# Performance work log

Hardware: AMD Instinct MI355X
Metric: run time of the kernel (lower is better)

The kernel has to match this reference:

```python
import jax, jax.numpy as jnp
import numpy as np

# dims
B, S, A = 16384, 300, 30
EMB, M_TOK, M_PROTO = 256, 8, 16
H_ENC, H_DEC, MF, NZ = 256, 128, 12, 4
ALPHA_MIN, ALPHA_MAX, ETA0 = 0.06, 0.3, 0.1
TECH_IDX = jnp.array([61, 91, 121, 151, 181, 211, 241, 271])


def setup_inputs() -> dict:
    key = jax.random.key(0)
    ks = jax.random.split(key, 20)
    def w(k, shape, fan):
        return jax.random.normal(k, shape, jnp.float32) * (fan ** -0.5)
    return {
        'state':   jax.random.uniform(ks[0], (B, S), jnp.float32),
        'fitness': jax.random.uniform(ks[1], (B, M_PROTO), jnp.float32),
        'proto_keys': jax.random.normal(ks[2], (M_PROTO, EMB), jnp.float32) * (EMB ** -0.5),
        'enc_W1': w(ks[3], (S, H_ENC), S),   'enc_b1': jnp.zeros((H_ENC,), jnp.float32),
        'ln_g':   jnp.ones((H_ENC,), jnp.float32), 'ln_b': jnp.zeros((H_ENC,), jnp.float32),
        'enc_W2': w(ks[4], (H_ENC, M_TOK * EMB), H_ENC), 'enc_b2': jnp.zeros((M_TOK * EMB,), jnp.float32),
        'dec_W1': w(ks[5], (M_PROTO, EMB, H_DEC), EMB),  'dec_b1': jnp.zeros((M_PROTO, H_DEC), jnp.float32),
        'dec_W2': w(ks[6], (M_PROTO, H_DEC, A), H_DEC),  'dec_b2': jnp.zeros((M_PROTO, A), jnp.float32),
        'tc_W':  w(ks[7], (MF, EMB), MF),  'tc_b':  jnp.zeros((EMB,), jnp.float32),
        'tc_cW': w(ks[8], (EMB, 1), EMB),  'tc_cb': jnp.zeros((1,), jnp.float32),
        'tc_zW': w(ks[9], (EMB, NZ), EMB), 'tc_zb': jnp.zeros((NZ,), jnp.float32),
        'w_prev': jnp.full((1, M_PROTO), 1.0 / M_PROTO, jnp.float32),
    }


def _layernorm(x, g, b, eps=1e-5):
    mu = x.mean(-1, keepdims=True)
    var = ((x - mu) ** 2).mean(-1, keepdims=True)
    return (x - mu) * jax.lax.rsqrt(var + eps) * g + b


def _forward(state, fitness, proto_keys, enc_W1, enc_b1, ln_g, ln_b, enc_W2, enc_b2,
             dec_W1, dec_b1, dec_W2, dec_b2, tc_W, tc_b, tc_cW, tc_cb, tc_zW, tc_zb, w_prev):
    # --- market feature extraction ---
    balance = state[:, 0:1]
    prices = state[:, 1:31]
    shares = state[:, 31:61]
    price_mean = prices.mean(1, keepdims=True)
    price_std = jnp.std(prices, axis=1, keepdims=True, ddof=1) + 1e-8  # torch.std is unbiased
    total_value = balance + (prices * shares).sum(1, keepdims=True)
    cash_ratio = balance / (total_value + 1e-8)
    tech = state[:, TECH_IDX]
    mf = jnp.concatenate([balance, price_mean, price_std, cash_ratio, tech], axis=1)  # [B,12]
    # --- T-Cell (minimal surrogate: danger embed, crisis level, crisis types) ---
    danger = jnp.tanh(mf @ tc_W + tc_b)                     # [B,EMB]
    crisis = jax.nn.sigmoid(danger @ tc_cW + tc_cb)         # [B,1]
    z = jax.nn.softmax(danger @ tc_zW + tc_zb, axis=-1)     # [B,NZ]
    # --- epitope encoder: Linear -> LN -> ReLU -> Linear -> reshape [B,m,EMB] ---
    h = jax.nn.relu(_layernorm(state @ enc_W1 + enc_b1, ln_g, ln_b))
    E = (h @ enc_W2 + enc_b2).reshape(-1, M_TOK, EMB)
    # --- IRT routing (OT-attention + fitness replicator, crisis-gated mix) ---
    scale = EMB ** -0.5
    logits = jnp.einsum('bme,ne->bmn', E, proto_keys) * scale \
           + (jnp.einsum('be,ne->bn', danger, proto_keys) * scale)[:, None, :]  # [B,m,M]
    P = jax.nn.softmax(logits, axis=-1)
    w_ot = P.mean(axis=1)                                   # [B,M]
    w_rep = w_prev * jnp.exp(ETA0 * fitness)
    w_rep = w_rep / (w_rep.sum(-1, keepdims=True) + 1e-8)
    alpha_c = ALPHA_MIN + (ALPHA_MAX - ALPHA_MIN) * (1.0 - crisis)  # [B,1]
    w = alpha_c * w_ot + (1.0 - alpha_c) * w_rep
    w = w / (w.sum(-1, keepdims=True) + 1e-8)
    # --- per-expert decoders on proto_keys (batched GEMM over M experts) ---
    hd = jax.nn.relu(jnp.einsum('me,meh->mh', proto_keys, dec_W1) + dec_b1)
    conc = jax.nn.softplus(jnp.einsum('mh,mha->ma', hd, dec_W2) + dec_b2)  # [M,A]
    mixed = jnp.einsum('bm,ma->ba', w, conc) + 1.0          # [B,A]
    # deterministic branch: softmax action head
    action = jax.nn.softmax(mixed, axis=-1)
    action = jnp.clip(action, 0.0, 1.0)
    action = action / (action.sum(-1, keepdims=True) + 1e-8)
    return action


def reference(state, fitness, proto_keys, enc_W1, enc_b1, ln_g, ln_b, enc_W2, enc_b2,
              dec_W1, dec_b1, dec_W2, dec_b2, tc_W, tc_b, tc_cW, tc_cb, tc_zW, tc_zb, w_prev):
    return _forward(state, fitness, proto_keys, enc_W1, enc_b1, ln_g, ln_b, enc_W2, enc_b2,
                    dec_W1, dec_b1, dec_W2, dec_b2, tc_W, tc_b, tc_cW, tc_cb, tc_zW, tc_zb, w_prev)
```

## Files before the change

kernel.cpp:

```cpp
#include <hip/hip_runtime.h>

typedef __attribute__((ext_vector_type(8))) short bf16x8;
typedef __attribute__((ext_vector_type(4))) float f32x4;

#define NBATCH 16384
#define SS     300
#define AA     30
#define ROWS   16
#define SSTR   352
#define HSTR   280
#define LSTR   132
#define K1P    320
#define SCALEF 0.0625f
#define ETA0   0.1f

__device__ __forceinline__ short f2b(float x) {
    unsigned u = __float_as_uint(x);
    unsigned r = (u + 0x7FFFu + ((u >> 16) & 1u)) >> 16;
    return (short)r;
}
__device__ __forceinline__ float b2f(short s) {
    return __uint_as_float(((unsigned)(unsigned short)s) << 16);
}
__device__ __forceinline__ float tanh_fast(float x) {
    float e = __expf(2.f * x);
    return 1.f - 2.f / (e + 1.f);
}

__global__ __launch_bounds__(256) void pre_kernel(
    const float* __restrict__ proto, const float* __restrict__ W1,
    const float* __restrict__ W2,   const float* __restrict__ b2,
    const float* __restrict__ tcW,  const float* __restrict__ cWp,
    const float* __restrict__ dW1,  const float* __restrict__ db1,
    const float* __restrict__ dW2,  const float* __restrict__ db2,
    short* __restrict__ W1P, short* __restrict__ W3P,
    short* __restrict__ PDP, short* __restrict__ TCP,
    float* __restrict__ cmn, float* __restrict__ conc)
{
    __shared__ short sbuf[64 * 264 + 4096];
    const int t = threadIdx.x;
    const int bid = blockIdx.x;

    if (bid < 32) {
        const int m = bid >> 2, jt = bid & 3;
        short* W2s = sbuf;
        short* prS = sbuf + 64 * 264;
        #pragma unroll 8
        for (int it = 0; it < 64; ++it) {
            const int idx = it * 256 + t, j = idx >> 8, e = idx & 255;
            W2s[j * 264 + e] = f2b(W2[(size_t)(jt * 64 + j) * 2048 + m * 256 + e]);
        }
        #pragma unroll 8
        for (int it = 0; it < 16; ++it) {
            const int id = it * 256 + t, chunk = id >> 3, j8 = id & 7;
            const int kt = chunk >> 6, rem = chunk & 63, q = rem >> 4, n = rem & 15;
            prS[id] = f2b(proto[n * 256 + kt * 32 + q * 8 + j8]);
        }
        __syncthreads();
        const int lane = t & 63, wv = t >> 6, l15 = lane & 15, q = lane >> 4;
        f32x4 acc = {0.f, 0.f, 0.f, 0.f};
        for (int kt = 0; kt < 8; ++kt) {
            bf16x8 a = *(const bf16x8*)&W2s[(wv * 16 + l15) * 264 + kt * 32 + q * 8];
            bf16x8 b = *(const bf16x8*)&prS[((kt * 4 + q) * 16 + l15) * 8];
            acc = __builtin_amdgcn_mfma_f32_16x16x32_bf16(a, b, acc, 0, 0, 0);
        }
        #pragma unroll
        for (int reg = 0; reg < 4; ++reg) {
            const int jg = jt * 64 + wv * 16 + q * 4 + reg;
            const int c = m * 16 + l15;
            const int ktj = jg >> 5, qj = (jg >> 3) & 3, j8 = jg & 7;
            W3P[((ktj * 4 + qj) * 128 + c) * 8 + j8] = f2b(acc[reg]);
        }
    } else if (bid < 42) {
        const int kt = bid - 32;
        short* W1s = sbuf;
        #pragma unroll 8
        for (int it = 0; it < 32; ++it) {
            const int idx = it * 256 + t, k = idx >> 8, n = idx & 255;
            const int kg = kt * 32 + k;
            W1s[k * 256 + n] = (kg < SS) ? f2b(W1[(size_t)kg * 256 + n]) : (short)0;
        }
        __syncthreads();
        #pragma unroll
        for (int it = 0; it < 4; ++it) {
            const int id = it * 256 + t, q = id >> 8, n = id & 255;
            bf16x8 v;
            #pragma unroll
            for (int j = 0; j < 8; ++j) v[j] = W1s[(q * 8 + j) * 256 + n];
            *(bf16x8*)&W1P[((kt * 4 + q) * 256 + n) * 8] = v;
        }
    } else if (bid == 42) {
        #pragma unroll 4
        for (int it = 0; it < 32; ++it) {
            const int id = it * 256 + t, chunk = id >> 3, j8 = id & 7;
            const int kt = chunk >> 7, q = (chunk >> 5) & 3, np = chunk & 31;
            const int k = kt * 32 + q * 8 + j8;
            float v = 0.f;
            if (np < 16) v = proto[np * 256 + k];
            else if (np == 16) v = cWp[k];
            PDP[id] = f2b(v);
        }
    } else if (bid == 43) {
        #pragma unroll 4
        for (int it = 0; it < 32; ++it) {
            const int id = it * 256 + t, chunk = id >> 3, j8 = id & 7;
            const int q = chunk >> 8, n = chunk & 255, k = q * 8 + j8;
            TCP[id] = (k < 12) ? f2b(tcW[k * 256 + n]) : (short)0;
        }
    } else if (bid == 44) {
        float* b2s = (float*)sbuf;
        float* prF = b2s + 2048;
        #pragma unroll
        for (int it = 0; it < 8; ++it)  b2s[it * 256 + t] = b2[it * 256 + t];
        #pragma unroll
        for (int it = 0; it < 16; ++it) prF[it * 256 + t] = proto[it * 256 + t];
        __syncthreads();
        if (t < 128) {
            const int mq = t >> 4, n = t & 15;
            float acc = 0.f;
            #pragma unroll 4
            for (int e = 0; e < 256; ++e) acc += b2s[mq * 256 + e] * prF[n * 256 + e];
            cmn[t] = acc;
        }
    } else {
        const int m = bid - 45;
        float* pr    = (float*)sbuf;
        float* hdp   = pr + 256;
        float* hdv   = hdp + 256;
        float* cpart = hdv + 128;
        pr[t] = proto[m * 256 + t];
        __syncthreads();
        {
            const int half = t >> 7, h = t & 127;
            const float* wp = dW1 + (size_t)m * 32768 + (size_t)half * 16384 + h;
            float a0 = 0.f, a1 = 0.f, a2 = 0.f, a3 = 0.f;
            #pragma unroll 8
            for (int e = 0; e < 128; e += 4) {
                const int eg = half * 128 + e;
                a0 = fmaf(pr[eg + 0], wp[(e + 0) * 128], a0);
                a1 = fmaf(pr[eg + 1], wp[(e + 1) * 128], a1);
                a2 = fmaf(pr[eg + 2], wp[(e + 2) * 128], a2);
                a3 = fmaf(pr[eg + 3], wp[(e + 3) * 128], a3);
            }
            hdp[half * 128 + h] = (a0 + a1) + (a2 + a3);
        }
        __syncthreads();
        if (t < 128) hdv[t] = fmaxf(hdp[t] + hdp[128 + t] + db1[m * 128 + t], 0.f);
        __syncthreads();
        {
            const int g = t >> 5, a = t & 31;
            float cacc = 0.f;
            if (a < AA) {
                const float* w2p = dW2 + (size_t)m * 128 * AA + g * 16 * AA + a;
                #pragma unroll
                for (int hh = 0; hh < 16; ++hh)
                    cacc = fmaf(hdv[g * 16 + hh], w2p[hh * AA], cacc);
            }
            cpart[g * 32 + a] = cacc;
        }
        __syncthreads();
        if (t < AA) {
            float s = db2[m * AA + t];
            #pragma unroll
            for (int g2 = 0; g2 < 8; ++g2) s += cpart[g2 * 32 + t];
            conc[m * AA + t] = fmaxf(s, 0.f) + log1pf(__expf(-fabsf(s)));
        }
    }
}

__global__ __launch_bounds__(256, 5) void main_kernel(
    const float* __restrict__ state, const float* __restrict__ fitness,
    const float* __restrict__ b1,
    const float* __restrict__ lng,  const float* __restrict__ lnb,
    const float* __restrict__ tcb,  const float* __restrict__ cb,
    const float* __restrict__ pw,
    const short* __restrict__ W1P,  const short* __restrict__ W3P,
    const short* __restrict__ PDP,  const short* __restrict__ TCP,
    const float* __restrict__ cmn,  const float* __restrict__ conc,
    float* __restrict__ out)
{
    const int t    = threadIdx.x;
    const int row0 = blockIdx.x * ROWS;
    const int w    = t >> 6;
    const int lane = t & 63;
    const int l15  = lane & 15;
    const int q    = lane >> 4;

    __shared__ short sA[ROWS * SSTR];
    __shared__ short sB[ROWS * HSTR];
    __shared__ short s_mfB[ROWS * 32];
    __shared__ float s_red[ROWS][8];
    __shared__ float s_mu[ROWS], s_rstd[ROWS];
    __shared__ float s_dd[ROWS * 16];
    __shared__ float s_crisis[ROWS];
    __shared__ float s_cmn[128];
    __shared__ float s_conc[16 * AA];

    float* s_log  = (float*)sB;
    float* s_wrep = (float*)&sA[ROWS * HSTR];

    #pragma unroll 4
    for (int it = 0; it < 20; ++it) {
        const int idx = it * 256 + t, r = idx / K1P, k = idx - r * K1P;
        sA[r * SSTR + k] = (k < SS) ? f2b(state[(size_t)(row0 + r) * SS + k]) : (short)0;
    }
    for (int it = t; it < 128 + 16 * AA; it += 256) {
        if (it < 128) s_cmn[it] = cmn[it];
        else s_conc[it - 128] = conc[it - 128];
    }
    __syncthreads();

    {
        const int r = t >> 4, g = t & 15;
        float sp = 0.f, sp2 = 0.f, sps = 0.f;
        if (g < 15) {
            #pragma unroll
            for (int jj = 0; jj < 2; ++jj) {
                const int i = 2 * g + jj;
                const float p = b2f(sA[r * SSTR + 1 + i]);
                const float s = b2f(sA[r * SSTR + 31 + i]);
                sp += p; sp2 += p * p; sps += p * s;
            }
        }
        #pragma unroll
        for (int off = 1; off < 16; off <<= 1) {
            sp  += __shfl_xor(sp, off);
            sp2 += __shfl_xor(sp2, off);
            sps += __shfl_xor(sps, off);
        }
        if (g < 8) s_mfB[r * 32 + 4 + g] = sA[r * SSTR + 61 + 30 * g];
        for (int k = 12 + g; k < 32; k += 16) s_mfB[r * 32 + k] = 0;
        if (g == 0) {
            const float bal = b2f(sA[r * SSTR]);
            const float pm = sp * (1.f / 30.f);
            const float var = (sp2 - 30.f * pm * pm) * (1.f / 29.f);
            const float pstd = sqrtf(fmaxf(var, 0.f)) + 1e-8f;
            s_mfB[r * 32 + 0] = sA[r * SSTR];
            s_mfB[r * 32 + 1] = f2b(pm);
            s_mfB[r * 32 + 2] = f2b(pstd);
            s_mfB[r * 32 + 3] = f2b(bal / (bal + sps + 1e-8f));
        }
    }
    __syncthreads();

    {
        f32x4 dacc[4];
        #pragma unroll
        for (int u = 0; u < 4; ++u) dacc[u] = (f32x4){0.f, 0.f, 0.f, 0.f};
        bf16x8 a = *(const bf16x8*)&s_mfB[l15 * 32 + q * 8];
        #pragma unroll
        for (int u = 0; u < 4; ++u) {
            bf16x8 b = *(const bf16x8*)&TCP[((q << 8) | (w * 64 + u * 16 + l15)) * 8];
            dacc[u] = __builtin_amdgcn_mfma_f32_16x16x32_bf16(a, b, dacc[u], 0, 0, 0);
        }
        #pragma unroll
        for (int u = 0; u < 4; ++u) {
            const int col = w * 64 + u * 16 + l15;
            const float tb = tcb[col];
            #pragma unroll
            for (int reg = 0; reg < 4; ++reg)
                sB[(q * 4 + reg) * HSTR + col] = f2b(tanh_fast(dacc[u][reg] + tb));
        }
    }
    __syncthreads();

    if (w == 0) {
        f32x4 acc = {0.f, 0.f, 0.f, 0.f};
        for (int kt = 0; kt < 8; ++kt) {
            bf16x8 a = *(const bf16x8*)&sB[l15 * HSTR + kt * 32 + q * 8];
            bf16x8 b = *(const bf16x8*)&PDP[((kt * 4 + q) * 32 + l15) * 8];
            acc = __builtin_amdgcn_mfma_f32_16x16x32_bf16(a, b, acc, 0, 0, 0);
        }
        #pragma unroll
        for (int reg = 0; reg < 4; ++reg)
            s_dd[(q * 4 + reg) * 16 + l15] = acc[reg];
    } else if (w == 1) {
        f32x4 acc = {0.f, 0.f, 0.f, 0.f};
        for (int kt = 0; kt < 8; ++kt) {
            bf16x8 a = *(const bf16x8*)&sB[l15 * HSTR + kt * 32 + q * 8];
            bf16x8 b = *(const bf16x8*)&PDP[((kt * 4 + q) * 32 + 16 + l15) * 8];
            acc = __builtin_amdgcn_mfma_f32_16x16x32_bf16(a, b, acc, 0, 0, 0);
        }
        if (l15 == 0) {
            const float cbv = cb[0];
            #pragma unroll
            for (int reg = 0; reg < 4; ++reg)
                s_crisis[q * 4 + reg] = 1.f / (1.f + __expf(-(acc[reg] + cbv)));
        }
    }

    f32x4 acc[4];
    #pragma unroll
    for (int u = 0; u < 4; ++u) acc[u] = (f32x4){0.f, 0.f, 0.f, 0.f};
    for (int kt = 0; kt < 10; ++kt) {
        bf16x8 a = *(const bf16x8*)&sA[l15 * SSTR + kt * 32 + q * 8];
        bf16x8 bfr[4];
        #pragma unroll
        for (int u = 0; u < 4; ++u)
            bfr[u] = *(const bf16x8*)&W1P[((kt * 4 + q) * 256 + (w * 64 + u * 16 + l15)) * 8];
        #pragma unroll
        for (int u = 0; u < 4; ++u)
            acc[u] = __builtin_amdgcn_mfma_f32_16x16x32_bf16(a, bfr[u], acc[u], 0, 0, 0);
    }

    {
        float b1v[4];
        #pragma unroll
        for (int u = 0; u < 4; ++u) b1v[u] = b1[w * 64 + u * 16 + l15];
        #pragma unroll
        for (int reg = 0; reg < 4; ++reg) {
            float s = 0.f, s2 = 0.f;
            #pragma unroll
            for (int u = 0; u < 4; ++u) {
                const float v = acc[u][reg] + b1v[u];
                acc[u][reg] = v;
                s += v; s2 += v * v;
            }
            #pragma unroll
            for (int off = 1; off < 16; off <<= 1) {
                s  += __shfl_xor(s, off);
                s2 += __shfl_xor(s2, off);
            }
            if (l15 == 0) {
                const int row = q * 4 + reg;
                s_red[row][w * 2]     = s;
                s_red[row][w * 2 + 1] = s2;
            }
        }
    }
    __syncthreads();
    if (t < ROWS) {
        float S = 0.f, S2 = 0.f;
        #pragma unroll
        for (int ww = 0; ww < 4; ++ww) { S += s_red[t][2 * ww]; S2 += s_red[t][2 * ww + 1]; }
        const float mu = S * (1.f / 256.f);
        const float var = S2 * (1.f / 256.f) - mu * mu;
        s_mu[t] = mu; s_rstd[t] = rsqrtf(var + 1e-5f);
    }
    __syncthreads();

    {
        float gv[4], bv[4];
        #pragma unroll
        for (int u = 0; u < 4; ++u) {
            gv[u] = lng[w * 64 + u * 16 + l15];
            bv[u] = lnb[w * 64 + u * 16 + l15];
        }
        #pragma unroll
        for (int reg = 0; reg < 4; ++reg) {
            const int row = q * 4 + reg;
            const float mu = s_mu[row], rs = s_rstd[row];
            #pragma unroll
            for (int u = 0; u < 4; ++u) {
                const int col = w * 64 + u * 16 + l15;
                const float v = fmaxf((acc[u][reg] - mu) * rs * gv[u] + bv[u], 0.f);
                sA[row * HSTR + col] = f2b(v);
            }
        }
    }
    __syncthreads();

    {
        f32x4 c2[2];
        c2[0] = (f32x4){0.f, 0.f, 0.f, 0.f};
        c2[1] = (f32x4){0.f, 0.f, 0.f, 0.f};
        for (int kt = 0; kt < 8; ++kt) {
            bf16x8 a = *(const bf16x8*)&sA[l15 * HSTR + kt * 32 + q * 8];
            bf16x8 b0 = *(const bf16x8*)&W3P[((kt * 4 + q) * 128 + w * 32 + l15) * 8];
            bf16x8 b1f = *(const bf16x8*)&W3P[((kt * 4 + q) * 128 + w * 32 + 16 + l15) * 8];
            c2[0] = __builtin_amdgcn_mfma_f32_16x16x32_bf16(a, b0, c2[0], 0, 0, 0);
            c2[1] = __builtin_amdgcn_mfma_f32_16x16x32_bf16(a, b1f, c2[1], 0, 0, 0);
        }
        const float cm0 = s_cmn[w * 32 + l15], cm1 = s_cmn[w * 32 + 16 + l15];
        #pragma unroll
        for (int reg = 0; reg < 4; ++reg) {
            const int row = q * 4 + reg;
            const float dd = s_dd[row * 16 + l15];
            s_log[row * LSTR + w * 32 + l15]      = SCALEF * (c2[0][reg] + cm0 + dd);
            s_log[row * LSTR + w * 32 + 16 + l15] = SCALEF * (c2[1][reg] + cm1 + dd);
        }
    }
    __syncthreads();

    if (t < 128) {
        const int r = t >> 3, m = t & 7;
        float* lg = &s_log[r * LSTR + m * 16];
        float mx = lg[0];
        #pragma unroll
        for (int n = 1; n < 16; ++n) mx = fmaxf(mx, lg[n]);
        float sum = 0.f, p[16];
        #pragma unroll
        for (int n = 0; n < 16; ++n) { p[n] = __expf(lg[n] - mx); sum += p[n]; }
        const float inv = 1.f / sum;
        #pragma unroll
        for (int n = 0; n < 16; ++n) lg[n] = p[n] * inv;
    }
    __syncthreads();

    {
        const int r = t >> 4, n = t & 15;
        float wot = 0.f;
        #pragma unroll
        for (int m = 0; m < 8; ++m) wot += s_log[r * LSTR + m * 16 + n];
        s_dd[t] = wot * 0.125f;
        s_wrep[t] = pw[n] * __expf(ETA0 * fitness[(size_t)(row0 + r) * 16 + n]);
    }
    __syncthreads();

    if (t < ROWS) {
        float srep = 0.f;
        #pragma unroll
        for (int n = 0; n < 16; ++n) srep += s_wrep[t * 16 + n];
        const float irep = 1.f / (srep + 1e-8f);
        const float alpha = 0.06f + 0.24f * (1.f - s_crisis[t]);
        float wn[16], sw = 0.f;
        #pragma unroll
        for (int n = 0; n < 16; ++n) {
            wn[n] = alpha * s_dd[t * 16 + n] + (1.f - alpha) * s_wrep[t * 16 + n] * irep;
            sw += wn[n];
        }
        const float isw = 1.f / (sw + 1e-8f);
        #pragma unroll
        for (int n = 0; n < 16; ++n) s_dd[t * 16 + n] = wn[n] * isw;
    }
    __syncthreads();

    {
        const int r = w * 4 + q;
        const int a0 = l15;
        const int a1 = a0 + 16;
        const bool v1 = a1 < AA;
        float wreg[16];
        #pragma unroll
        for (int n = 0; n < 16; ++n) wreg[n] = s_dd[r * 16 + n];
        float m0 = 1.f, m1 = 1.f;
        const int a1s = v1 ? a1 : 0;
        #pragma unroll
        for (int n = 0; n < 16; ++n) {
            m0 = fmaf(wreg[n], s_conc[n * AA + a0], m0);
            m1 = fmaf(wreg[n], s_conc[n * AA + a1s], m1);
        }
        float mx = v1 ? fmaxf(m0, m1) : m0;
        #pragma unroll
        for (int off = 1; off < 16; off <<= 1) mx = fmaxf(mx, __shfl_xor(mx, off));
        float e0 = __expf(m0 - mx);
        float e1 = v1 ? __expf(m1 - mx) : 0.f;
        float se = e0 + e1;
        #pragma unroll
        for (int off = 1; off < 16; off <<= 1) se += __shfl_xor(se, off);
        const float inv = 1.f / se;
        out[(size_t)(row0 + r) * AA + a0] = e0 * inv;
        if (v1) out[(size_t)(row0 + r) * AA + a1] = e1 * inv;
    }
}

extern "C" void kernel_launch(void* const* d_in, const int* in_sizes, int n_in,
                              void* d_out, int out_size, void* d_ws, size_t ws_size,
                              hipStream_t stream) {
    const float* state   = (const float*)d_in[0];
    const float* fitness = (const float*)d_in[1];
    const float* proto   = (const float*)d_in[2];
    const float* enc_W1  = (const float*)d_in[3];
    const float* enc_b1  = (const float*)d_in[4];
    const float* ln_g    = (const float*)d_in[5];
    const float* ln_b    = (const float*)d_in[6];
    const float* enc_W2  = (const float*)d_in[7];
    const float* enc_b2  = (const float*)d_in[8];
    const float* dec_W1  = (const float*)d_in[9];
    const float* dec_b1  = (const float*)d_in[10];
    const float* dec_W2  = (const float*)d_in[11];
    const float* dec_b2  = (const float*)d_in[12];
    const float* tc_W    = (const float*)d_in[13];
    const float* tc_b    = (const float*)d_in[14];
    const float* tc_cW   = (const float*)d_in[15];
    const float* tc_cb   = (const float*)d_in[16];
    const float* w_prev  = (const float*)d_in[19];
    float* out = (float*)d_out;

    short* W1P = (short*)d_ws;
    short* W3P = W1P + 81920;
    short* PDP = W3P + 32768;
    short* TCP = PDP + 8192;
    float* cmn  = (float*)(TCP + 8192);
    float* conc = cmn + 128;

    pre_kernel<<<61, 256, 0, stream>>>(proto, enc_W1, enc_W2, enc_b2,
                                       tc_W, tc_cW,
                                       dec_W1, dec_b1, dec_W2, dec_b2,
                                       W1P, W3P, PDP, TCP, cmn, conc);
    main_kernel<<<NBATCH / ROWS, 256, 0, stream>>>(state, fitness,
                                                   enc_b1, ln_g, ln_b,
                                                   tc_b, tc_cb, w_prev,
                                                   W1P, W3P, PDP, TCP, cmn, conc, out);
}
```

Measured before the change: 132.8 us.

## Vectorize state load, prefetch fitness, overlap W1 GEMM, drop LN barrier

The state tile is now loaded as float4 with packed bf16 stores, and the shared row stride is shrunk to fit. Fitness and prior weights are prefetched at kernel entry so their global latency is hidden. The encoder W1 GEMM moves ahead of the barrier so it runs alongside the tech-context stage, and each thread recomputes the LayerNorm mean and rstd from the partial sums, removing one shared round trip and one __syncthreads. This costs extra register pressure and redundant per-thread reductions.

```diff
diff --git a/kernel.cpp b/kernel.cpp
--- a/kernel.cpp
+++ b/kernel.cpp
@@ -7,7 +7,7 @@
 #define SS     300
 #define AA     30
 #define ROWS   16
-#define SSTR   352
+#define SSTR   328
 #define HSTR   280
 #define LSTR   132
 #define K1P    320
@@ -190,7 +190,6 @@
     __shared__ short sB[ROWS * HSTR];
     __shared__ short s_mfB[ROWS * 32];
     __shared__ float s_red[ROWS][8];
-    __shared__ float s_mu[ROWS], s_rstd[ROWS];
     __shared__ float s_dd[ROWS * 16];
     __shared__ float s_crisis[ROWS];
     __shared__ float s_cmn[128];
@@ -199,10 +198,23 @@
     float* s_log  = (float*)sB;
     float* s_wrep = (float*)&sA[ROWS * HSTR];
 
-    #pragma unroll 4
-    for (int it = 0; it < 20; ++it) {
-        const int idx = it * 256 + t, r = idx / K1P, k = idx - r * K1P;
-        sA[r * SSTR + k] = (k < SS) ? f2b(state[(size_t)(row0 + r) * SS + k]) : (short)0;
+    const float fit_pre = fitness[(size_t)(row0 + (t >> 4)) * 16 + (t & 15)];
+    const float pw_pre  = pw[t & 15];
+
+    #pragma unroll
+    for (int it = 0; it < 5; ++it) {
+        const int idx = it * 256 + t;
+        if (idx < ROWS * 75) {
+            const int r = idx / 75, c4 = idx - r * 75;
+            const float4 v = *(const float4*)&state[(size_t)(row0 + r) * SS + c4 * 4];
+            short4 s4;
+            s4.x = f2b(v.x); s4.y = f2b(v.y); s4.z = f2b(v.z); s4.w = f2b(v.w);
+            *(short4*)&sA[r * SSTR + c4 * 4] = s4;
+        }
+    }
+    for (int i = t; i < ROWS * 20; i += 256) {
+        const int r = i / 20, k = SS + i - r * 20;
+        sA[r * SSTR + k] = 0;
     }
     for (int it = t; it < 128 + 16 * AA; it += 256) {
         if (it < 128) s_cmn[it] = cmn[it];
@@ -243,15 +255,16 @@
     }
     __syncthreads();
 
+    f32x4 acc[4];
     {
         f32x4 dacc[4];
         #pragma unroll
         for (int u = 0; u < 4; ++u) dacc[u] = (f32x4){0.f, 0.f, 0.f, 0.f};
-        bf16x8 a = *(const bf16x8*)&s_mfB[l15 * 32 + q * 8];
+        bf16x8 amf = *(const bf16x8*)&s_mfB[l15 * 32 + q * 8];
         #pragma unroll
         for (int u = 0; u < 4; ++u) {
             bf16x8 b = *(const bf16x8*)&TCP[((q << 8) | (w * 64 + u * 16 + l15)) * 8];
-            dacc[u] = __builtin_amdgcn_mfma_f32_16x16x32_bf16(a, b, dacc[u], 0, 0, 0);
+            dacc[u] = __builtin_amdgcn_mfma_f32_16x16x32_bf16(amf, b, dacc[u], 0, 0, 0);
         }
         #pragma unroll
         for (int u = 0; u < 4; ++u) {
@@ -261,48 +274,45 @@
             for (int reg = 0; reg < 4; ++reg)
                 sB[(q * 4 + reg) * HSTR + col] = f2b(tanh_fast(dacc[u][reg] + tb));
         }
+        #pragma unroll
+        for (int u = 0; u < 4; ++u) acc[u] = (f32x4){0.f, 0.f, 0.f, 0.f};
+        for (int kt = 0; kt < 10; ++kt) {
+            bf16x8 a = *(const bf16x8*)&sA[l15 * SSTR + kt * 32 + q * 8];
+            bf16x8 bfr[4];
+            #pragma unroll
+            for (int u = 0; u < 4; ++u)
+                bfr[u] = *(const bf16x8*)&W1P[((kt * 4 + q) * 256 + (w * 64 + u * 16 + l15)) * 8];
+            #pragma unroll
+            for (int u = 0; u < 4; ++u)
+                acc[u] = __builtin_amdgcn_mfma_f32_16x16x32_bf16(a, bfr[u], acc[u], 0, 0, 0);
+        }
     }
     __syncthreads();
 
     if (w == 0) {
-        f32x4 acc = {0.f, 0.f, 0.f, 0.f};
+        f32x4 ad = {0.f, 0.f, 0.f, 0.f};
         for (int kt = 0; kt < 8; ++kt) {
             bf16x8 a = *(const bf16x8*)&sB[l15 * HSTR + kt * 32 + q * 8];
             bf16x8 b = *(const bf16x8*)&PDP[((kt * 4 + q) * 32 + l15) * 8];
-            acc = __builtin_amdgcn_mfma_f32_16x16x32_bf16(a, b, acc, 0, 0, 0);
+            ad = __builtin_amdgcn_mfma_f32_16x16x32_bf16(a, b, ad, 0, 0, 0);
         }
         #pragma unroll
         for (int reg = 0; reg < 4; ++reg)
-            s_dd[(q * 4 + reg) * 16 + l15] = acc[reg];
+            s_dd[(q * 4 + reg) * 16 + l15] = ad[reg];
     } else if (w == 1) {
-        f32x4 acc = {0.f, 0.f, 0.f, 0.f};
+        f32x4 ad = {0.f, 0.f, 0.f, 0.f};
         for (int kt = 0; kt < 8; ++kt) {
             bf16x8 a = *(const bf16x8*)&sB[l15 * HSTR + kt * 32 + q * 8];
             bf16x8 b = *(const bf16x8*)&PDP[((kt * 4 + q) * 32 + 16 + l15) * 8];
-            acc = __builtin_amdgcn_mfma_f32_16x16x32_bf16(a, b, acc, 0, 0, 0);
+            ad = __builtin_amdgcn_mfma_f32_16x16x32_bf16(a, b, ad, 0, 0, 0);
         }
         if (l15 == 0) {
             const float cbv = cb[0];
             #pragma unroll
             for (int reg = 0; reg < 4; ++reg)
-                s_crisis[q * 4 + reg] = 1.f / (1.f + __expf(-(acc[reg] + cbv)));
-        }
-    }
-
-    f32x4 acc[4];
-    #pragma unroll
-    for (int u = 0; u < 4; ++u) acc[u] = (f32x4){0.f, 0.f, 0.f, 0.f};
-    for (int kt = 0; kt < 10; ++kt) {
-        bf16x8 a = *(const bf16x8*)&sA[l15 * SSTR + kt * 32 + q * 8];
-        bf16x8 bfr[4];
-        #pragma unroll
-        for (int u = 0; u < 4; ++u)
-            bfr[u] = *(const bf16x8*)&W1P[((kt * 4 + q) * 256 + (w * 64 + u * 16 + l15)) * 8];
-        #pragma unroll
-        for (int u = 0; u < 4; ++u)
-            acc[u] = __builtin_amdgcn_mfma_f32_16x16x32_bf16(a, bfr[u], acc[u], 0, 0, 0);
-    }
-
+                s_crisis[q * 4 + reg] = 1.f / (1.f + __expf(-(ad[reg] + cbv)));
+        }
+    }
     {
         float b1v[4];
         #pragma unroll
@@ -329,15 +339,18 @@
         }
     }
     __syncthreads();
-    if (t < ROWS) {
+
+    float muv[4], rsv[4];
+    #pragma unroll
+    for (int reg = 0; reg < 4; ++reg) {
+        const int row = q * 4 + reg;
         float S = 0.f, S2 = 0.f;
         #pragma unroll
-        for (int ww = 0; ww < 4; ++ww) { S += s_red[t][2 * ww]; S2 += s_red[t][2 * ww + 1]; }
+        for (int ww = 0; ww < 4; ++ww) { S += s_red[row][2 * ww]; S2 += s_red[row][2 * ww + 1]; }
         const float mu = S * (1.f / 256.f);
         const float var = S2 * (1.f / 256.f) - mu * mu;
-        s_mu[t] = mu; s_rstd[t] = rsqrtf(var + 1e-5f);
-    }
-    __syncthreads();
+        muv[reg] = mu; rsv[reg] = rsqrtf(var + 1e-5f);
+    }
 
     {
         float gv[4], bv[4];
@@ -349,11 +362,10 @@
         #pragma unroll
         for (int reg = 0; reg < 4; ++reg) {
             const int row = q * 4 + reg;
-            const float mu = s_mu[row], rs = s_rstd[row];
             #pragma unroll
             for (int u = 0; u < 4; ++u) {
                 const int col = w * 64 + u * 16 + l15;
-                const float v = fmaxf((acc[u][reg] - mu) * rs * gv[u] + bv[u], 0.f);
+                const float v = fmaxf((acc[u][reg] - muv[reg]) * rsv[reg] * gv[u] + bv[u], 0.f);
                 sA[row * HSTR + col] = f2b(v);
             }
         }
@@ -398,12 +410,12 @@
     __syncthreads();
 
     {
-        const int r = t >> 4, n = t & 15;
+        const int r = t >> 4;
         float wot = 0.f;
         #pragma unroll
-        for (int m = 0; m < 8; ++m) wot += s_log[r * LSTR + m * 16 + n];
+        for (int m = 0; m < 8; ++m) wot += s_log[r * LSTR + m * 16 + (t & 15)];
         s_dd[t] = wot * 0.125f;
-        s_wrep[t] = pw[n] * __expf(ETA0 * fitness[(size_t)(row0 + r) * 16 + n]);
+        s_wrep[t] = pw_pre * __expf(ETA0 * fit_pre);
     }
     __syncthreads();
 
```

After: 128.5 us (median of 2 runs). 1.03x faster.
